# Performance work log

Measured on AMD Instinct MI355X. Metric: run time of the kernel, lower is better.

The kernel has to match this reference:

```python
import jax, jax.numpy as jnp
import numpy as np
import math

B, N, C, A, H = 1, 320, 128, 32, 4  # batch, n_res, rep_2d channels, attn channels, heads


def _layernorm(x, w, b, eps=1e-5):
    mu = jnp.mean(x, axis=-1, keepdims=True)
    var = jnp.var(x, axis=-1, keepdims=True)
    return (x - mu) * jax.lax.rsqrt(var + eps) * w + b


def setup_inputs() -> dict:
    key = jax.random.key(0)
    ks = jax.random.split(key, 12)
    s = 0.02
    return {
        "x2d": jax.random.normal(ks[0], (B, N, N, C), dtype=jnp.float32),
        "mask": jnp.ones((B, N, N), dtype=jnp.float32),
        "norm_w": jnp.ones((C,), dtype=jnp.float32),
        "norm_b": jnp.zeros((C,), dtype=jnp.float32),
        "Wq": jax.random.normal(ks[1], (C, A * H), dtype=jnp.float32) * s,
        "Wk": jax.random.normal(ks[2], (C, A * H), dtype=jnp.float32) * s,
        "Wv": jax.random.normal(ks[3], (C, A * H), dtype=jnp.float32) * s,
        "Wb": jax.random.normal(ks[4], (C, H), dtype=jnp.float32) * s,
        "Wg": jax.random.normal(ks[5], (C, A * H), dtype=jnp.float32) * s,
        "bg": jnp.zeros((A * H,), dtype=jnp.float32),
        "Wo": jax.random.normal(ks[6], (A * H, C), dtype=jnp.float32) * s,
        "bo": jnp.zeros((C,), dtype=jnp.float32),
    }


def reference(x2d, mask, norm_w, norm_b, Wq, Wk, Wv, Wb, Wg, bg, Wo, bo):
    xn = _layernorm(x2d, norm_w, norm_b)                      # [B,N,N,C]
    # note: torch .view(..., A, H) splits the output channel as (A, H)
    q = (xn @ Wq).reshape(B, N, N, A, H)
    k = (xn @ Wk).reshape(B, N, N, A, H)
    v = (xn @ Wv).reshape(B, N, N, A, H)
    b = xn @ Wb                                               # [B,N,N,H] -> b[b,j,k,h]
    g = jax.nn.sigmoid((xn @ Wg + bg).reshape(B, N, N, A, H))
    w = jnp.einsum('bijch,bikch->bijkh', q, k) / math.sqrt(A)
    # torch: b.unsqueeze(1).transpose(2,3) => w[b,i,j,k,h] += b[b,k,j,h]
    w = w + jnp.transpose(b, (0, 2, 1, 3))[:, None]           # [B,1,N,N,H]
    w = (w + 100.0) * mask[:, :, None, :, None] - 100.0
    w = jax.nn.softmax(w, axis=-2)                            # over k
    out = jnp.einsum('bijkh,bikch->bijch', w, v) * g          # [B,N,N,A,H]
    out = out.reshape(B, N, N, A * H) @ Wo + bo               # [B,N,N,C]
    out = out * mask[..., None]
    return out
```

## Files before the change

kernel.cpp:

```cpp
#include <hip/hip_runtime.h>
#include <hip/hip_bf16.h>
#include <math.h>

#define N 320
#define C 128
#define A 32
#define H 4
#define NPOS (N*N)

typedef __attribute__((ext_vector_type(8))) __bf16 bf16x8;
typedef __attribute__((ext_vector_type(16))) float f32x16;

union frag_u { int4 i; bf16x8 v; unsigned u[4]; };

#define MFMA32(va, vb, vc) __builtin_amdgcn_mfma_f32_32x32x16_bf16((va), (vb), (vc), 0, 0, 0)

#define WAVE_LDS_FENCE() do { \
    asm volatile("s_waitcnt lgkmcnt(0)" ::: "memory"); \
    __builtin_amdgcn_sched_barrier(0); \
} while (0)

static __device__ __forceinline__ unsigned pk_bf16(float lo, float hi) {
    union { __hip_bfloat162 h; unsigned u; } cv;
    cv.h = __float22bfloat162_rn(make_float2(lo, hi));
    return cv.u;
}

static __device__ __forceinline__ float bf16_to_f32(unsigned short u) {
    union { unsigned u; float f; } c;
    c.u = ((unsigned)u) << 16;
    return c.f;
}

__global__ __launch_bounds__(256)
void wprep_kernel(const float* __restrict__ Wq,
                  const float* __restrict__ Wk,
                  const float* __restrict__ Wv,
                  const float* __restrict__ Wg,
                  const float* __restrict__ Wo,
                  unsigned short* __restrict__ WF) {
    const float isq = 0.17677669529663687f;
    int tid = blockIdx.x * 256 + threadIdx.x;
    int lane = tid & 63;
    int kk = (tid >> 6) & 7;
    int ct = (tid >> 9) & 3;
    int mat = tid >> 11;
    const float* src = (mat == 0) ? Wq : (mat == 1) ? Wk : (mat == 2) ? Wv
                     : (mat == 3) ? Wg : Wo;
    float scl = (mat == 0) ? isq : 1.0f;
    int col = ct * 32 + (lane & 31);
    int c0 = kk * 16 + (lane >> 5) * 8;
    float v[8];
    #pragma unroll
    for (int e = 0; e < 8; e++) {
        int rr = c0 + e;
        int srow = (mat == 4) ? (((rr & 31) << 2) | (rr >> 5)) : rr;
        v[e] = src[(size_t)srow * 128 + col] * scl;
    }
    int4 out;
    out.x = pk_bf16(v[0], v[1]);
    out.y = pk_bf16(v[2], v[3]);
    out.z = pk_bf16(v[4], v[5]);
    out.w = pk_bf16(v[6], v[7]);
    *(int4*)((char*)WF + (size_t)tid * 16) = out;
}

__global__ __launch_bounds__(256)
void btrans_kernel(const float* __restrict__ Bp, float* __restrict__ BpT) {
    __shared__ float tile[64][65];
    const int b = blockIdx.x;
    const int h = b / 25;
    const int bk = (b % 25) / 5;
    const int bj = b % 5;
    const int k0 = bk * 64, j0 = bj * 64;
    const float* src = Bp + (size_t)h * NPOS;
    float* dst = BpT + (size_t)h * NPOS;
    const int t = threadIdx.x;
    #pragma unroll
    for (int u = 0; u < 16; ++u) {
        int idx = u * 256 + t;
        int kk = idx >> 6, jj = idx & 63;
        tile[kk][jj] = src[(size_t)(k0 + kk) * N + j0 + jj];
    }
    __syncthreads();
    #pragma unroll
    for (int u = 0; u < 16; ++u) {
        int idx = u * 256 + t;
        int jj = idx >> 6, kk = idx & 63;
        dst[(size_t)(j0 + jj) * N + k0 + kk] = tile[kk][jj];
    }
}

__global__ __launch_bounds__(256)
void ln_proj_kernel(const float* __restrict__ x2d,
                    const float* __restrict__ norm_w,
                    const float* __restrict__ norm_b,
                    const float* __restrict__ Wb,
                    const float* __restrict__ bg,
                    const unsigned short* __restrict__ WF,
                    unsigned short* __restrict__ Qb,
                    unsigned short* __restrict__ Kb,
                    unsigned short* __restrict__ Vta,
                    unsigned short* __restrict__ Gb,
                    float* __restrict__ Bp) {
    __shared__ __align__(16) unsigned char shbuf[33280];
    unsigned char* xnb = shbuf;

    const int t = threadIdx.x;
    const int gpos0 = blockIdx.x * 64;

    {
        const int r = t >> 2, s = t & 3;
        const float4* src = (const float4*)(x2d + (size_t)(gpos0 + r) * 128 + s * 32);
        float4 xv[8];
        #pragma unroll
        for (int u = 0; u < 8; u++) xv[u] = src[u];
        float sum = 0.f, sq = 0.f;
        #pragma unroll
        for (int u = 0; u < 8; u++) {
            sum += xv[u].x + xv[u].y + xv[u].z + xv[u].w;
            sq += xv[u].x * xv[u].x + xv[u].y * xv[u].y
                + xv[u].z * xv[u].z + xv[u].w * xv[u].w;
        }
        sum += __shfl_xor(sum, 1); sum += __shfl_xor(sum, 2);
        sq  += __shfl_xor(sq, 1);  sq  += __shfl_xor(sq, 2);
        float mean = sum * (1.0f / 128.0f);
        float var  = sq * (1.0f / 128.0f) - mean * mean;
        float rstd = rsqrtf(var + 1e-5f);

        const float4* wsrc = (const float4*)(norm_w + s * 32);
        const float4* bsrc = (const float4*)(norm_b + s * 32);
        const float4* wb4  = (const float4*)Wb;
        float pb0 = 0.f, pb1 = 0.f, pb2 = 0.f, pb3 = 0.f;
        float4 xe;
        #pragma unroll
        for (int u = 0; u < 8; u++) {
            float4 wv = wsrc[u], bv = bsrc[u], x4 = xv[u];
            float4 xn;
            xn.x = (x4.x - mean) * rstd * wv.x + bv.x;
            xn.y = (x4.y - mean) * rstd * wv.y + bv.y;
            xn.z = (x4.z - mean) * rstd * wv.z + bv.z;
            xn.w = (x4.w - mean) * rstd * wv.w + bv.w;
            int cb = s * 32 + u * 4;
            float4 w0 = wb4[cb + 0], w1 = wb4[cb + 1], w2 = wb4[cb + 2], w3 = wb4[cb + 3];
            pb0 = fmaf(xn.x, w0.x, fmaf(xn.y, w1.x, fmaf(xn.z, w2.x, fmaf(xn.w, w3.x, pb0))));
            pb1 = fmaf(xn.x, w0.y, fmaf(xn.y, w1.y, fmaf(xn.z, w2.y, fmaf(xn.w, w3.y, pb1))));
            pb2 = fmaf(xn.x, w0.z, fmaf(xn.y, w1.z, fmaf(xn.z, w2.z, fmaf(xn.w, w3.z, pb2))));
            pb3 = fmaf(xn.x, w0.w, fmaf(xn.y, w1.w, fmaf(xn.z, w2.w, fmaf(xn.w, w3.w, pb3))));
            if (u & 1) {
                int g = s * 4 + (u >> 1);
                int4 gr;
                gr.x = pk_bf16(xe.x, xe.y);
                gr.y = pk_bf16(xe.z, xe.w);
                gr.z = pk_bf16(xn.x, xn.y);
                gr.w = pk_bf16(xn.z, xn.w);
                *(int4*)(xnb + r * 256 + ((g ^ (r & 7)) << 4)) = gr;
            } else {
                xe = xn;
            }
        }
        pb0 += __shfl_xor(pb0, 1); pb0 += __shfl_xor(pb0, 2);
        pb1 += __shfl_xor(pb1, 1); pb1 += __shfl_xor(pb1, 2);
        pb2 += __shfl_xor(pb2, 1); pb2 += __shfl_xor(pb2, 2);
        pb3 += __shfl_xor(pb3, 1); pb3 += __shfl_xor(pb3, 2);
        float pbsel = (s == 0) ? pb0 : (s == 1) ? pb1 : (s == 2) ? pb2 : pb3;
        Bp[(size_t)s * NPOS + gpos0 + r] = pbsel;
    }
    __syncthreads();

    const int lane = t & 63;
    const int w = t >> 6;
    const int col = lane & 31;
    const int hi = lane >> 5;

    frag_u af[2][8];
    #pragma unroll
    for (int rt = 0; rt < 2; rt++)
        #pragma unroll
        for (int kk = 0; kk < 8; kk++) {
            int row = rt * 32 + col;
            af[rt][kk].i = *(const int4*)(xnb + row * 256 + (((kk * 2 + hi) ^ (row & 7)) << 4));
        }
    __syncthreads();

    const char* wf = (const char*)WF + (size_t)w * 4 * 8 * 1024;
    float* stage_w = (float*)shbuf + w * 2080;

    for (int ct = 0; ct < 4; ct++) {
        f32x16 acc0, acc1;
        #pragma unroll
        for (int r = 0; r < 16; r++) { acc0[r] = 0.f; acc1[r] = 0.f; }
        #pragma unroll
        for (int kk = 0; kk < 8; kk++) {
            frag_u bf;
            bf.i = *(const int4*)(wf + (ct * 8 + kk) * 1024 + lane * 16);
            acc0 = MFMA32(af[0][kk].v, bf.v, acc0);
            acc1 = MFMA32(af[1][kk].v, bf.v, acc1);
        }
        #pragma unroll
        for (int r = 0; r < 16; r++) {
            int patr = (r & 3) + 8 * (r >> 2) + 4 * hi;
            stage_w[col * 65 + patr] = acc0[r];
            stage_w[col * 65 + 32 + patr] = acc1[r];
        }
        WAVE_LDS_FENCE();
        if (w < 2) {
            char* dst = (w == 0) ? (char*)Qb : (char*)Kb;
            #pragma unroll
            for (int h = 0; h < 4; h++) {
                float f[8];
                #pragma unroll
                for (int u = 0; u < 8; u++) f[u] = stage_w[(u * 4 + h) * 65 + lane];
                int4 val;
                val.x = pk_bf16(f[0], f[1]);
                val.y = pk_bf16(f[2], f[3]);
                val.z = pk_bf16(f[4], f[5]);
                val.w = pk_bf16(f[6], f[7]);
                *(int4*)(dst + ((size_t)(h * 4 + ct) * NPOS + gpos0 + lane) * 16) = val;
            }
        } else if (w == 2) {
            int cc = lane & 31, half = lane >> 5;
            int plane = (cc & 3) * 32 + ct * 8 + (cc >> 2);
            unsigned pk[16];
            #pragma unroll
            for (int j2 = 0; j2 < 16; j2++)
                pk[j2] = pk_bf16(stage_w[cc * 65 + half * 32 + 2 * j2],
                                 stage_w[cc * 65 + half * 32 + 2 * j2 + 1]);
            int4* dst = (int4*)((char*)Vta + ((size_t)plane * NPOS + gpos0 + half * 32) * 2);
            dst[0] = make_int4(pk[0], pk[1], pk[2], pk[3]);
            dst[1] = make_int4(pk[4], pk[5], pk[6], pk[7]);
            dst[2] = make_int4(pk[8], pk[9], pk[10], pk[11]);
            dst[3] = make_int4(pk[12], pk[13], pk[14], pk[15]);
        } else {
            #pragma unroll
            for (int h = 0; h < 4; h++) {
                float f[8];
                #pragma unroll
                for (int u = 0; u < 8; u++) {
                    float z = stage_w[(u * 4 + h) * 65 + lane] + bg[ct * 32 + u * 4 + h];
                    f[u] = 1.0f / (1.0f + __expf(-z));
                }
                int4 val;
                val.x = pk_bf16(f[0], f[1]);
                val.y = pk_bf16(f[2], f[3]);
                val.z = pk_bf16(f[4], f[5]);
                val.w = pk_bf16(f[6], f[7]);
                *(int4*)((char*)Gb + ((size_t)(h * 4 + ct) * NPOS + gpos0 + lane) * 16) = val;
            }
        }
        WAVE_LDS_FENCE();
    }
}

__global__ __launch_bounds__(320, 2)
void attn_kernel(const unsigned short* __restrict__ Qb,
                 const unsigned short* __restrict__ Kb,
                 const unsigned short* __restrict__ Vta,
                 const unsigned short* __restrict__ Gb,
                 const float* __restrict__ BpT,
                 const float* __restrict__ mask,
                 unsigned short* __restrict__ Ob) {
    __shared__ __align__(16) unsigned char smem[40960];
    __shared__ float mparr[320];
    __shared__ float m2arr[320];
    unsigned char* Klds = smem;
    unsigned char* Vlds = smem + 20480;

    const int i = blockIdx.x >> 2;
    const int h = blockIdx.x & 3;
    const int t = threadIdx.x;
    const int lane = t & 63;
    const int w = t >> 6;
    const int col = lane & 31;
    const int hi = lane >> 5;
    const int jt0 = w * 64;

    frag_u qf[2][2];
    const char* qplane = (const char*)Qb + ((size_t)(h * 4) * NPOS + (size_t)i * N) * 16;
    #pragma unroll
    for (int jt = 0; jt < 2; ++jt) {
        int jrow = jt0 + jt * 32 + col;
        #pragma unroll
        for (int cf = 0; cf < 2; ++cf) {
            int g = cf * 2 + hi;
            qf[jt][cf].i = *(const int4*)(qplane + ((size_t)g * NPOS + jrow) * 16);
        }
    }

    const char* kplane = (const char*)Kb + ((size_t)(h * 4) * NPOS + (size_t)i * N) * 16;
    #pragma unroll
    for (int it = 0; it < 4; ++it) {
        int4 val = *(const int4*)(kplane + ((size_t)it * NPOS + t) * 16);
        *(int4*)(Klds + t * 64 + ((it ^ ((t >> 1) & 3)) << 4)) = val;
    }
    const char* vbsrc = (const char*)Vta + ((size_t)h * 32 * NPOS + (size_t)i * N) * 2;
    #pragma unroll
    for (int it = 0; it < 4; ++it) {
        int tt = t + it * 320;
        int a = tt / 40, kg = tt % 40;
        int4 val = *(const int4*)(vbsrc + (size_t)a * NPOS * 2 + kg * 16);
        *(int4*)(Vlds + a * 640 + ((kg ^ (a & 7)) << 4)) = val;
    }
    {
        int kt_ = t >> 5, hi_ = (t >> 4) & 1, r_ = t & 15;
        int k = kt_ * 32 + (r_ & 3) + 8 * (r_ >> 2) + 4 * hi_;
        float m_ = mask[(size_t)i * N + k];
        mparr[t] = m_;
        m2arr[t] = fmaf(100.f, m_, -100.f);
    }
    __syncthreads();

    f32x16 accO[2];
    #pragma unroll
    for (int r = 0; r < 16; ++r) { accO[0][r] = 0.f; accO[1][r] = 0.f; }
    float lsum[2] = { 0.f, 0.f };

    const float* br0 = BpT + (size_t)h * NPOS + (size_t)(jt0 + col) * N + 4 * hi;
    const float* br1 = br0 + (size_t)32 * N;

    float4 b0[4], b1[4];
    #pragma unroll
    for (int q = 0; q < 4; ++q) b0[q] = *(const float4*)(br0 + 8 * q);

#define PROCESS_JT(JT, BB)                                                      \
    {                                                                           \
        f32x16 S;                                                               \
        _Pragma("unroll") for (int r = 0; r < 16; ++r) S[r] = 0.f;              \
        __builtin_amdgcn_s_setprio(1);                                          \
        S = MFMA32(kf0.v, qf[JT][0].v, S);                                      \
        S = MFMA32(kf1.v, qf[JT][1].v, S);                                      \
        __builtin_amdgcn_s_setprio(0);                                          \
        float pe[16];                                                           \
        float l0 = 0.f, l1 = 0.f, l2 = 0.f, l3 = 0.f;                           \
        _Pragma("unroll") for (int q = 0; q < 4; ++q) {                         \
            float sv0 = fmaf(S[4*q+0] + BB[q].x, mk4[q].x, m2v[q].x);           \
            float sv1 = fmaf(S[4*q+1] + BB[q].y, mk4[q].y, m2v[q].y);           \
            float sv2 = fmaf(S[4*q+2] + BB[q].z, mk4[q].z, m2v[q].z);           \
            float sv3 = fmaf(S[4*q+3] + BB[q].w, mk4[q].w, m2v[q].w);           \
            pe[4*q+0] = __expf(sv0); pe[4*q+1] = __expf(sv1);                   \
            pe[4*q+2] = __expf(sv2); pe[4*q+3] = __expf(sv3);                   \
            l0 += pe[4*q+0]; l1 += pe[4*q+1];                                   \
            l2 += pe[4*q+2]; l3 += pe[4*q+3];                                   \
        }                                                                       \
        lsum[JT] += (l0 + l1) + (l2 + l3);                                      \
        unsigned p[8];                                                          \
        _Pragma("unroll") for (int q = 0; q < 8; ++q)                           \
            p[q] = pk_bf16(pe[2 * q], pe[2 * q + 1]);                           \
        unsigned x0 = p[0], y0 = p[2];                                          \
        unsigned x1 = p[1], y1 = p[3];                                          \
        unsigned x2 = p[4], y2 = p[6];                                          \
        unsigned x3 = p[5], y3 = p[7];                                          \
        asm("v_permlane32_swap_b32 %0, %1" : "+v"(x0), "+v"(y0));               \
        asm("v_permlane32_swap_b32 %0, %1" : "+v"(x1), "+v"(y1));               \
        asm("v_permlane32_swap_b32 %0, %1" : "+v"(x2), "+v"(y2));               \
        asm("v_permlane32_swap_b32 %0, %1" : "+v"(x3), "+v"(y3));               \
        frag_u bf0, bf1;                                                        \
        bf0.u[0] = x0; bf0.u[1] = x1; bf0.u[2] = y0; bf0.u[3] = y1;             \
        bf1.u[0] = x2; bf1.u[1] = x3; bf1.u[2] = y2; bf1.u[3] = y3;             \
        __builtin_amdgcn_s_setprio(1);                                          \
        accO[JT] = MFMA32(vf0.v, bf0.v, accO[JT]);                              \
        accO[JT] = MFMA32(vf1.v, bf1.v, accO[JT]);                              \
        __builtin_amdgcn_s_setprio(0);                                          \
    }

    for (int kt = 0; kt < 10; ++kt) {
        const int kbase = kt * 32;
        const int krow = kbase + col;
        frag_u kf0, kf1, vf0, vf1;
        kf0.i = *(const int4*)(Klds + krow * 64 + (((0 + hi) ^ ((krow >> 1) & 3)) << 4));
        kf1.i = *(const int4*)(Klds + krow * 64 + (((2 + hi) ^ ((krow >> 1) & 3)) << 4));
        vf0.i = *(const int4*)(Vlds + col * 640 + (((kt * 4 + 0 + hi) ^ (col & 7)) << 4));
        vf1.i = *(const int4*)(Vlds + col * 640 + (((kt * 4 + 2 + hi) ^ (col & 7)) << 4));

        float4 mk4[4], m2v[4];
        const float* mp  = mparr + kbase + hi * 16;
        const float* m2p = m2arr + kbase + hi * 16;
        #pragma unroll
        for (int q = 0; q < 4; ++q) {
            mk4[q] = *(const float4*)(mp + 4 * q);
            m2v[q] = *(const float4*)(m2p + 4 * q);
        }

        #pragma unroll
        for (int q = 0; q < 4; ++q) b1[q] = *(const float4*)(br1 + kbase + 8 * q);

        PROCESS_JT(0, b0)

        if (kt < 9) {
            #pragma unroll
            for (int q = 0; q < 4; ++q) b0[q] = *(const float4*)(br0 + kbase + 32 + 8 * q);
        }

        PROCESS_JT(1, b1)
    }
#undef PROCESS_JT

    __syncthreads();
    float* st = (float*)(smem + w * 8192);
    const char* gplane = (const char*)Gb + ((size_t)(h * 4) * NPOS + (size_t)i * N) * 16;

    #pragma unroll
    for (int jt = 0; jt < 2; ++jt) {
        float lt = lsum[jt] + __shfl_xor(lsum[jt], 32);
        float inv = 1.0f / lt;
        #pragma unroll
        for (int r = 0; r < 16; ++r) {
            const int a = (r & 3) + 8 * (r >> 2) + 4 * hi;
            st[col * 33 + a] = accO[jt][r] * inv;
        }
        WAVE_LDS_FENCE();
        {
            int jj = lane & 31;
            int ah0 = hi * 16;
            int jrow = jt0 + jt * 32 + jj;
            int4 g0 = *(const int4*)(gplane + ((size_t)(2 * hi + 0) * NPOS + jrow) * 16);
            int4 g1 = *(const int4*)(gplane + ((size_t)(2 * hi + 1) * NPOS + jrow) * 16);
            unsigned gw[8] = { (unsigned)g0.x, (unsigned)g0.y, (unsigned)g0.z, (unsigned)g0.w,
                               (unsigned)g1.x, (unsigned)g1.y, (unsigned)g1.z, (unsigned)g1.w };
            unsigned pk8[8];
            #pragma unroll
            for (int e = 0; e < 8; ++e) {
                float ge0 = bf16_to_f32((unsigned short)(gw[e] & 0xffffu));
                float ge1 = bf16_to_f32((unsigned short)(gw[e] >> 16));
                pk8[e] = pk_bf16(st[jj * 33 + ah0 + 2 * e + 0] * ge0,
                                 st[jj * 33 + ah0 + 2 * e + 1] * ge1);
            }
            char* dst = (char*)Ob + (((size_t)i * N + jrow) * 128 + h * 32 + ah0) * 2;
            *(int4*)dst = make_int4(pk8[0], pk8[1], pk8[2], pk8[3]);
            *(int4*)(dst + 16) = make_int4(pk8[4], pk8[5], pk8[6], pk8[7]);
        }
        WAVE_LDS_FENCE();
    }
}

__global__ __launch_bounds__(256)
void outproj_kernel(const unsigned short* __restrict__ Ob,
                    const unsigned short* __restrict__ WoF,
                    const float* __restrict__ bo,
                    const float* __restrict__ mask,
                    float* __restrict__ out) {
    __shared__ __align__(16) unsigned char obs[64 * 256];
    __shared__ float stage[4][32 * 65];

    const int t = threadIdx.x;
    const int gpos0 = blockIdx.x * 64;

    {
        const int r = t >> 2, s = t & 3;
        const char* src = (const char*)Ob + ((size_t)(gpos0 + r) * 128 + s * 32) * 2;
        #pragma unroll
        for (int u = 0; u < 4; ++u) {
            int4 v = *(const int4*)(src + u * 16);
            int g = s * 4 + u;
            *(int4*)(obs + r * 256 + ((g ^ (r & 7)) << 4)) = v;
        }
    }
    __syncthreads();

    const int lane = t & 63;
    const int w = t >> 6;
    const int col = lane & 31;
    const int hi = lane >> 5;

    f32x16 acc0, acc1;
    float bocol = bo[w * 32 + col];
    #pragma unroll
    for (int r = 0; r < 16; ++r) { acc0[r] = bocol; acc1[r] = bocol; }

    const char* wf = (const char*)WoF + (size_t)w * 8 * 1024;
    #pragma unroll
    for (int kk = 0; kk < 8; ++kk) {
        frag_u bf, a0, a1;
        bf.i = *(const int4*)(wf + kk * 1024 + lane * 16);
        int row0 = col, row1 = 32 + col;
        a0.i = *(const int4*)(obs + row0 * 256 + (((kk * 2 + hi) ^ (row0 & 7)) << 4));
        a1.i = *(const int4*)(obs + row1 * 256 + (((kk * 2 + hi) ^ (row1 & 7)) << 4));
        acc0 = MFMA32(a0.v, bf.v, acc0);
        acc1 = MFMA32(a1.v, bf.v, acc1);
    }

    float* st = stage[w];
    #pragma unroll
    for (int r = 0; r < 16; ++r) {
        int patr = (r & 3) + 8 * (r >> 2) + 4 * hi;
        st[col * 65 + patr] = acc0[r];
        st[col * 65 + 32 + patr] = acc1[r];
    }
    WAVE_LDS_FENCE();
    {
        int row = lane;
        float mv = mask[gpos0 + row];
        float4* dst = (float4*)(out + (size_t)(gpos0 + row) * 128 + w * 32);
        #pragma unroll
        for (int u = 0; u < 8; ++u) {
            float4 o;
            o.x = st[(4 * u + 0) * 65 + row] * mv;
            o.y = st[(4 * u + 1) * 65 + row] * mv;
            o.z = st[(4 * u + 2) * 65 + row] * mv;
            o.w = st[(4 * u + 3) * 65 + row] * mv;
            dst[u] = o;
        }
    }
}

extern "C" void kernel_launch(void* const* d_in, const int* in_sizes, int n_in,
                              void* d_out, int out_size, void* d_ws, size_t ws_size,
                              hipStream_t stream) {
    const float* x2d    = (const float*)d_in[0];
    const float* mask   = (const float*)d_in[1];
    const float* norm_w = (const float*)d_in[2];
    const float* norm_b = (const float*)d_in[3];
    const float* Wq     = (const float*)d_in[4];
    const float* Wk     = (const float*)d_in[5];
    const float* Wv     = (const float*)d_in[6];
    const float* Wb     = (const float*)d_in[7];
    const float* Wg     = (const float*)d_in[8];
    const float* bg     = (const float*)d_in[9];
    const float* Wo     = (const float*)d_in[10];
    const float* bo     = (const float*)d_in[11];
    float* out = (float*)d_out;

    char* ws = (char*)d_ws;
    float* Bp  = (float*)ws;                                   ws += (size_t)H * NPOS * 4;
    float* BpT = (float*)ws;                                   ws += (size_t)H * NPOS * 4;
    unsigned short* Qb  = (unsigned short*)ws;                 ws += (size_t)NPOS * C * 2;
    unsigned short* Kb  = (unsigned short*)ws;                 ws += (size_t)NPOS * C * 2;
    unsigned short* Vta = (unsigned short*)ws;                 ws += (size_t)NPOS * C * 2;
    unsigned short* Gb  = (unsigned short*)ws;                 ws += (size_t)NPOS * C * 2;
    unsigned short* Ob  = (unsigned short*)ws;                 ws += (size_t)NPOS * C * 2;
    unsigned short* WF  = (unsigned short*)ws;
    unsigned short* WoF = WF + (size_t)4 * 16384;

    wprep_kernel<<<40, 256, 0, stream>>>(Wq, Wk, Wv, Wg, Wo, WF);

    ln_proj_kernel<<<NPOS / 64, 256, 0, stream>>>(x2d, norm_w, norm_b, Wb, bg,
                                                  WF, Qb, Kb, Vta, Gb, Bp);

    btrans_kernel<<<H * 25, 256, 0, stream>>>(Bp, BpT);

    attn_kernel<<<N * H, 320, 0, stream>>>(Qb, Kb, Vta, Gb, BpT, mask, Ob);

    outproj_kernel<<<NPOS / 64, 256, 0, stream>>>(Ob, WoF, bo, mask, out);
}
```

Baseline: 201.3 us.

## Halve ln_proj row tile to 32 positions per block for more blocks

The LayerNorm plus projection kernel now handles 32 positions per block instead of 64, with 8 threads per row and one MFMA accumulator per wave. Grid size doubles and LDS use roughly halves, which should raise occupancy and spread the work across more CUs. In exchange each weight fragment load feeds only one MFMA instead of two, halving weight reuse, and the global stores become narrower 8-byte writes.

Result: faster. 182.3 us (median of 2 runs) (-9.5%).

```diff
diff --git a/kernel.cpp b/kernel.cpp
--- a/kernel.cpp
+++ b/kernel.cpp
@@ -103,52 +103,52 @@
                     unsigned short* __restrict__ Vta,
                     unsigned short* __restrict__ Gb,
                     float* __restrict__ Bp) {
-    __shared__ __align__(16) unsigned char shbuf[33280];
+    __shared__ __align__(16) unsigned char shbuf[16896];
     unsigned char* xnb = shbuf;
 
     const int t = threadIdx.x;
-    const int gpos0 = blockIdx.x * 64;
+    const int gpos0 = blockIdx.x * 32;
 
     {
-        const int r = t >> 2, s = t & 3;
-        const float4* src = (const float4*)(x2d + (size_t)(gpos0 + r) * 128 + s * 32);
-        float4 xv[8];
-        #pragma unroll
-        for (int u = 0; u < 8; u++) xv[u] = src[u];
+        const int r = t >> 3, s = t & 7;
+        const float4* src = (const float4*)(x2d + (size_t)(gpos0 + r) * 128 + s * 16);
+        float4 xv[4];
+        #pragma unroll
+        for (int u = 0; u < 4; u++) xv[u] = src[u];
         float sum = 0.f, sq = 0.f;
         #pragma unroll
-        for (int u = 0; u < 8; u++) {
+        for (int u = 0; u < 4; u++) {
             sum += xv[u].x + xv[u].y + xv[u].z + xv[u].w;
             sq += xv[u].x * xv[u].x + xv[u].y * xv[u].y
                 + xv[u].z * xv[u].z + xv[u].w * xv[u].w;
         }
-        sum += __shfl_xor(sum, 1); sum += __shfl_xor(sum, 2);
-        sq  += __shfl_xor(sq, 1);  sq  += __shfl_xor(sq, 2);
+        sum += __shfl_xor(sum, 1); sum += __shfl_xor(sum, 2); sum += __shfl_xor(sum, 4);
+        sq  += __shfl_xor(sq, 1);  sq  += __shfl_xor(sq, 2);  sq  += __shfl_xor(sq, 4);
         float mean = sum * (1.0f / 128.0f);
         float var  = sq * (1.0f / 128.0f) - mean * mean;
         float rstd = rsqrtf(var + 1e-5f);
 
-        const float4* wsrc = (const float4*)(norm_w + s * 32);
-        const float4* bsrc = (const float4*)(norm_b + s * 32);
+        const float4* wsrc = (const float4*)(norm_w + s * 16);
+        const float4* bsrc = (const float4*)(norm_b + s * 16);
         const float4* wb4  = (const float4*)Wb;
         float pb0 = 0.f, pb1 = 0.f, pb2 = 0.f, pb3 = 0.f;
         float4 xe;
         #pragma unroll
-        for (int u = 0; u < 8; u++) {
+        for (int u = 0; u < 4; u++) {
             float4 wv = wsrc[u], bv = bsrc[u], x4 = xv[u];
             float4 xn;
             xn.x = (x4.x - mean) * rstd * wv.x + bv.x;
             xn.y = (x4.y - mean) * rstd * wv.y + bv.y;
             xn.z = (x4.z - mean) * rstd * wv.z + bv.z;
             xn.w = (x4.w - mean) * rstd * wv.w + bv.w;
-            int cb = s * 32 + u * 4;
+            int cb = s * 16 + u * 4;
             float4 w0 = wb4[cb + 0], w1 = wb4[cb + 1], w2 = wb4[cb + 2], w3 = wb4[cb + 3];
             pb0 = fmaf(xn.x, w0.x, fmaf(xn.y, w1.x, fmaf(xn.z, w2.x, fmaf(xn.w, w3.x, pb0))));
             pb1 = fmaf(xn.x, w0.y, fmaf(xn.y, w1.y, fmaf(xn.z, w2.y, fmaf(xn.w, w3.y, pb1))));
             pb2 = fmaf(xn.x, w0.z, fmaf(xn.y, w1.z, fmaf(xn.z, w2.z, fmaf(xn.w, w3.z, pb2))));
             pb3 = fmaf(xn.x, w0.w, fmaf(xn.y, w1.w, fmaf(xn.z, w2.w, fmaf(xn.w, w3.w, pb3))));
             if (u & 1) {
-                int g = s * 4 + (u >> 1);
+                int g = s * 2 + (u >> 1);
                 int4 gr;
                 gr.x = pk_bf16(xe.x, xe.y);
                 gr.y = pk_bf16(xe.z, xe.w);
@@ -159,12 +159,14 @@
                 xe = xn;
             }
         }
-        pb0 += __shfl_xor(pb0, 1); pb0 += __shfl_xor(pb0, 2);
-        pb1 += __shfl_xor(pb1, 1); pb1 += __shfl_xor(pb1, 2);
-        pb2 += __shfl_xor(pb2, 1); pb2 += __shfl_xor(pb2, 2);
-        pb3 += __shfl_xor(pb3, 1); pb3 += __shfl_xor(pb3, 2);
-        float pbsel = (s == 0) ? pb0 : (s == 1) ? pb1 : (s == 2) ? pb2 : pb3;
-        Bp[(size_t)s * NPOS + gpos0 + r] = pbsel;
+        pb0 += __shfl_xor(pb0, 1); pb0 += __shfl_xor(pb0, 2); pb0 += __shfl_xor(pb0, 4);
+        pb1 += __shfl_xor(pb1, 1); pb1 += __shfl_xor(pb1, 2); pb1 += __shfl_xor(pb1, 4);
+        pb2 += __shfl_xor(pb2, 1); pb2 += __shfl_xor(pb2, 2); pb2 += __shfl_xor(pb2, 4);
+        pb3 += __shfl_xor(pb3, 1); pb3 += __shfl_xor(pb3, 2); pb3 += __shfl_xor(pb3, 4);
+        if (s < 4) {
+            float pbsel = (s == 0) ? pb0 : (s == 1) ? pb1 : (s == 2) ? pb2 : pb3;
+            Bp[(size_t)s * NPOS + gpos0 + r] = pbsel;
+        }
     }
     __syncthreads();
 
@@ -173,79 +175,69 @@
     const int col = lane & 31;
     const int hi = lane >> 5;
 
-    frag_u af[2][8];
-    #pragma unroll
-    for (int rt = 0; rt < 2; rt++)
-        #pragma unroll
-        for (int kk = 0; kk < 8; kk++) {
-            int row = rt * 32 + col;
-            af[rt][kk].i = *(const int4*)(xnb + row * 256 + (((kk * 2 + hi) ^ (row & 7)) << 4));
-        }
+    frag_u af[8];
+    #pragma unroll
+    for (int kk = 0; kk < 8; kk++)
+        af[kk].i = *(const int4*)(xnb + col * 256 + (((kk * 2 + hi) ^ (col & 7)) << 4));
     __syncthreads();
 
     const char* wf = (const char*)WF + (size_t)w * 4 * 8 * 1024;
-    float* stage_w = (float*)shbuf + w * 2080;
+    float* stage_w = (float*)shbuf + w * 1056;
 
     for (int ct = 0; ct < 4; ct++) {
-        f32x16 acc0, acc1;
-        #pragma unroll
-        for (int r = 0; r < 16; r++) { acc0[r] = 0.f; acc1[r] = 0.f; }
+        f32x16 acc;
+        #pragma unroll
+        for (int r = 0; r < 16; r++) acc[r] = 0.f;
         #pragma unroll
         for (int kk = 0; kk < 8; kk++) {
             frag_u bf;
             bf.i = *(const int4*)(wf + (ct * 8 + kk) * 1024 + lane * 16);
-            acc0 = MFMA32(af[0][kk].v, bf.v, acc0);
-            acc1 = MFMA32(af[1][kk].v, bf.v, acc1);
+            acc = MFMA32(af[kk].v, bf.v, acc);
         }
         #pragma unroll
         for (int r = 0; r < 16; r++) {
             int patr = (r & 3) + 8 * (r >> 2) + 4 * hi;
-            stage_w[col * 65 + patr] = acc0[r];
-            stage_w[col * 65 + 32 + patr] = acc1[r];
+            stage_w[col * 33 + patr] = acc[r];
         }
         WAVE_LDS_FENCE();
         if (w < 2) {
             char* dst = (w == 0) ? (char*)Qb : (char*)Kb;
             #pragma unroll
             for (int h = 0; h < 4; h++) {
-                float f[8];
+                float f[4];
                 #pragma unroll
-                for (int u = 0; u < 8; u++) f[u] = stage_w[(u * 4 + h) * 65 + lane];
-                int4 val;
+                for (int e = 0; e < 4; e++)
+                    f[e] = stage_w[((hi * 4 + e) * 4 + h) * 33 + col];
+                uint2 val;
                 val.x = pk_bf16(f[0], f[1]);
                 val.y = pk_bf16(f[2], f[3]);
-                val.z = pk_bf16(f[4], f[5]);
-                val.w = pk_bf16(f[6], f[7]);
-                *(int4*)(dst + ((size_t)(h * 4 + ct) * NPOS + gpos0 + lane) * 16) = val;
+                *(uint2*)(dst + ((size_t)(h * 4 + ct) * NPOS + gpos0 + col) * 16 + hi * 8) = val;
             }
         } else if (w == 2) {
-            int cc = lane & 31, half = lane >> 5;
+            int cc = col, half = hi;
             int plane = (cc & 3) * 32 + ct * 8 + (cc >> 2);
-            unsigned pk[16];
+            unsigned pk[8];
             #pragma unroll
-            for (int j2 = 0; j2 < 16; j2++)
-                pk[j2] = pk_bf16(stage_w[cc * 65 + half * 32 + 2 * j2],
-                                 stage_w[cc * 65 + half * 32 + 2 * j2 + 1]);
-            int4* dst = (int4*)((char*)Vta + ((size_t)plane * NPOS + gpos0 + half * 32) * 2);
+            for (int j2 = 0; j2 < 8; j2++)
+                pk[j2] = pk_bf16(stage_w[cc * 33 + half * 16 + 2 * j2],
+                                 stage_w[cc * 33 + half * 16 + 2 * j2 + 1]);
+            int4* dst = (int4*)((char*)Vta + ((size_t)plane * NPOS + gpos0 + half * 16) * 2);
             dst[0] = make_int4(pk[0], pk[1], pk[2], pk[3]);
             dst[1] = make_int4(pk[4], pk[5], pk[6], pk[7]);
-            dst[2] = make_int4(pk[8], pk[9], pk[10], pk[11]);
-            dst[3] = make_int4(pk[12], pk[13], pk[14], pk[15]);
         } else {
             #pragma unroll
             for (int h = 0; h < 4; h++) {
-                float f[8];
+                float f[4];
                 #pragma unroll
-                for (int u = 0; u < 8; u++) {
-                    float z = stage_w[(u * 4 + h) * 65 + lane] + bg[ct * 32 + u * 4 + h];
-                    f[u] = 1.0f / (1.0f + __expf(-z));
+                for (int e = 0; e < 4; e++) {
+                    float z = stage_w[((hi * 4 + e) * 4 + h) * 33 + col]
+                            + bg[ct * 32 + (hi * 4 + e) * 4 + h];
+                    f[e] = 1.0f / (1.0f + __expf(-z));
                 }
-                int4 val;
+                uint2 val;
                 val.x = pk_bf16(f[0], f[1]);
                 val.y = pk_bf16(f[2], f[3]);
-                val.z = pk_bf16(f[4], f[5]);
-                val.w = pk_bf16(f[6], f[7]);
-                *(int4*)((char*)Gb + ((size_t)(h * 4 + ct) * NPOS + gpos0 + lane) * 16) = val;
+                *(uint2*)((char*)Gb + ((size_t)(h * 4 + ct) * NPOS + gpos0 + col) * 16 + hi * 8) = val;
             }
         }
         WAVE_LDS_FENCE();
@@ -533,7 +525,7 @@
 
     wprep_kernel<<<40, 256, 0, stream>>>(Wq, Wk, Wv, Wg, Wo, WF);
 
-    ln_proj_kernel<<<NPOS / 64, 256, 0, stream>>>(x2d, norm_w, norm_b, Wb, bg,
+    ln_proj_kernel<<<NPOS / 32, 256, 0, stream>>>(x2d, norm_w, norm_b, Wb, bg,
                                                   WF, Qb, Kb, Vta, Gb, Bp);
 
     btrans_kernel<<<H * 25, 256, 0, stream>>>(Bp, BpT);
```
